# Kernel optimization log

Hardware: AMD Instinct MI355X
Metric: run time of the kernel (lower is better)

The kernel has to match this reference:

```python
import jax, jax.numpy as jnp
import numpy as np

D_IN = 512
D_HID = D_IN // 2  # 256
D_OUT = 3


def setup_inputs() -> dict:
    key = jax.random.key(0)
    k_hs, k_ds, k1, k2, k3, k4 = jax.random.split(key, 6)
    B, L, Tmax = 16, 4096, 512
    hs = jax.random.normal(k_hs, (B, L, D_IN), dtype=jnp.float32)
    ds = jax.random.randint(k_ds, (B, Tmax), 0, 8, dtype=jnp.int64)
    # Linear params stored as (in, out); torch Linear does x @ W.T + b
    s1 = 1.0 / np.sqrt(D_IN)
    s2 = 1.0 / np.sqrt(D_HID)
    W1 = jax.random.uniform(k1, (D_IN, D_HID), jnp.float32, -s1, s1)
    b1 = jax.random.uniform(k2, (D_HID,), jnp.float32, -s1, s1)
    W2 = jax.random.uniform(k3, (D_HID, D_OUT), jnp.float32, -s2, s2)
    b2 = jax.random.uniform(k4, (D_OUT,), jnp.float32, -s2, s2)
    return {"hs": hs, "ds": ds, "W1": W1, "b1": b1, "W2": W2, "b2": b2, "Lmax": 4096}


def _align_durations(hs, ds, Lmax):
    # Vectorized equivalent of the per-element python loop:
    #   d_t = max(floor(ds[b,t] * L / Lmax), 1); segment mean over hs[b, i:i+d_t];
    #   i advances only when ds[b,t] > 0; rows with ds==0 stay zero.
    B, L, D = hs.shape
    mult = L / Lmax
    d = jnp.maximum(jnp.floor(ds.astype(jnp.float32) * mult).astype(jnp.int32), 1)
    valid = ds > 0
    d_eff = jnp.where(valid, d, 0)                      # (B, Tmax)
    starts = jnp.cumsum(d_eff, axis=1) - d_eff          # exclusive cumsum
    ends = starts + d_eff
    s_cl = jnp.clip(starts, 0, L)
    e_cl = jnp.clip(ends, 0, L)
    # prefix sums over frames: P[b, i] = sum of hs[b, :i]
    P = jnp.concatenate(
        [jnp.zeros((B, 1, D), hs.dtype), jnp.cumsum(hs, axis=1)], axis=1
    )  # (B, L+1, D)
    seg_sum = (jnp.take_along_axis(P, e_cl[:, :, None], axis=1)
               - jnp.take_along_axis(P, s_cl[:, :, None], axis=1))  # (B, Tmax, D)
    length = jnp.maximum(e_cl - s_cl, 1).astype(hs.dtype)
    mean = seg_sum / length[:, :, None]
    return jnp.where(valid[:, :, None], mean, jnp.zeros((), hs.dtype))


def reference(hs, ds, W1, b1, W2, b2, Lmax):
    aligned = _align_durations(hs, ds, Lmax)            # (B, Tmax, D_IN)
    # projection MLP (Dropout is identity in eval mode)
    h = jax.nn.relu(jnp.einsum("btd,dh->bth", aligned, W1) + b1)
    out = jax.nn.relu(jnp.einsum("bth,ho->bto", h, W2) + b2)
    return out
```

## Files before the change

### kernel.cpp

```cpp
#include <hip/hip_runtime.h>
#include <math.h>

#define BB    16
#define LL    4096
#define TMAX  512
#define DIN   512
#define DHID  256
#define DOUT  3
#define NROW  (BB * TMAX)
#define RPB   32
#define RPT   8

typedef __attribute__((ext_vector_type(8))) short bf16x8;
typedef __attribute__((ext_vector_type(4))) float f32x4;

static __device__ __forceinline__ ushort f2bf(float x) {
    uint u = __builtin_bit_cast(uint, x);
    u = (u + 0x7FFFu + ((u >> 16) & 1u)) >> 16;
    return (ushort)u;
}


__global__ __launch_bounds__(512) void prep_kernel(
    const int* __restrict__ ds, const int* __restrict__ lmax,
    const float* __restrict__ W1, int* __restrict__ starts,
    int* __restrict__ lens, ushort* __restrict__ pack) {
    __shared__ int   sbuf[TMAX];
    __shared__ float t[64][65];
    const int bid = blockIdx.x;
    const int tid = threadIdx.x;

    if (bid < BB) {
        const int b = bid;
        const float mult = (float)LL / (float)lmax[0];
        const int dsv = ds[b * TMAX + tid];
        int d = (int)floorf((float)dsv * mult);
        d = max(d, 1);
        const int deff = (dsv > 0) ? d : 0;
        sbuf[tid] = deff;
        __syncthreads();
        for (int off = 1; off < TMAX; off <<= 1) {
            int x = (tid >= off) ? sbuf[tid - off] : 0;
            __syncthreads();
            sbuf[tid] += x;
            __syncthreads();
        }
        starts[b * TMAX + tid] = sbuf[tid] - deff;
        lens[b * TMAX + tid]   = deff;
    } else {
        const int tb = bid - BB;
        const int k0 = (tb >> 2) * 64;
        const int n0 = (tb & 3) * 64;
        const int r  = tid >> 3;
        const int c8 = (tid & 7) * 8;
        #pragma unroll
        for (int i = 0; i < 2; ++i) {
            const float4 v =
                *(const float4*)&W1[(size_t)(k0 + r) * DHID + n0 + c8 + i * 4];
            t[r][c8 + i * 4 + 0] = v.x;
            t[r][c8 + i * 4 + 1] = v.y;
            t[r][c8 + i * 4 + 2] = v.z;
            t[r][c8 + i * 4 + 3] = v.w;
        }
        __syncthreads();
        const int col = n0 + r;
        const int kk  = k0 + c8;
        const int nb  = col >> 4;
        const int mm  = col & 15;
        const int ktc = kk >> 5;
        const int gg  = (kk >> 3) & 3;
        ushort tmp[8];
        #pragma unroll
        for (int j = 0; j < 8; ++j) tmp[j] = f2bf(t[c8 + j][r]);
        *(uint4*)&pack[(size_t)(((nb * 16 + ktc) * 64) + gg * 16 + mm) * 8] =
            *(const uint4*)tmp;
    }
}

__global__ __launch_bounds__(512, 2) void fused_kernel(
    const float* __restrict__ hs, const int* __restrict__ starts,
    const int* __restrict__ lens, const ushort* __restrict__ pack,
    const float* __restrict__ b1, const float* __restrict__ W2,
    const float* __restrict__ b2, float* __restrict__ out) {
    __shared__ ushort Asw[RPB * DIN];
    __shared__ float  red[8][RPB][DOUT];

    const int raw  = blockIdx.x;
    const int bid  = (raw & 7) * 32 + (raw >> 3);
    const int row0 = bid * RPB;
    const int b    = row0 >> 9;
    const int tid  = threadIdx.x;
    const int w    = tid >> 6;
    const int l    = tid & 63;
    const int m    = l & 15;
    const int g    = l >> 4;
    const int ct   = tid & 127;
    const int rh   = tid >> 7;

    int s_arr[RPT], n_arr[RPT], last_arr[RPT];
    int nmax = 0;
    #pragma unroll
    for (int rr = 0; rr < RPT; ++rr) {
        const int row = row0 + rh * RPT + rr;
        const int len = lens[row];
        int s = starts[row];
        int e = min(s + len, LL);
        s = min(s, LL);
        const int n = e - s;
        s_arr[rr]    = s;
        n_arr[rr]    = n;
        last_arr[rr] = min(max(e - 1, 0), LL - 1);
        nmax = max(nmax, n);
    }
    float4 a[RPT];
    #pragma unroll
    for (int rr = 0; rr < RPT; ++rr) a[rr] = make_float4(0.f, 0.f, 0.f, 0.f);

    const float* base = hs + (size_t)b * LL * DIN + ct * 4;
    for (int i = 0; i < nmax; ++i) {
        float4 v[RPT];
        #pragma unroll
        for (int rr = 0; rr < RPT; ++rr) {
            const int idx = min(s_arr[rr] + i, last_arr[rr]);
            v[rr] = *(const float4*)(base + (size_t)idx * DIN);
        }
        #pragma unroll
        for (int rr = 0; rr < RPT; ++rr) {
            const bool ok = (i < n_arr[rr]);
            a[rr].x += ok ? v[rr].x : 0.0f;
            a[rr].y += ok ? v[rr].y : 0.0f;
            a[rr].z += ok ? v[rr].z : 0.0f;
            a[rr].w += ok ? v[rr].w : 0.0f;
        }
    }
    #pragma unroll
    for (int rr = 0; rr < RPT; ++rr) {
        const int rl = rh * RPT + rr;
        const float inv = (n_arr[rr] > 0) ? 1.0f / (float)n_arr[rr] : 0.0f;
        ushort4 u;
        u.x = f2bf(a[rr].x * inv);
        u.y = f2bf(a[rr].y * inv);
        u.z = f2bf(a[rr].z * inv);
        u.w = f2bf(a[rr].w * inv);
        *(ushort4*)((char*)Asw + rl * 1024 + ((ct * 8) ^ ((rl & 7) << 4))) = u;
    }
    __syncthreads();

    f32x4 acc00 = {0.f, 0.f, 0.f, 0.f};
    f32x4 acc01 = {0.f, 0.f, 0.f, 0.f};
    f32x4 acc10 = {0.f, 0.f, 0.f, 0.f};
    f32x4 acc11 = {0.f, 0.f, 0.f, 0.f};

    const ushort* bb  = pack + (size_t)l * 8;
    const char* abase0 = (const char*)Asw + m * 1024;
    const char* abase1 = (const char*)Asw + (16 + m) * 1024;
    const int   aswz   = (m & 7) << 4;

    #pragma unroll 4
    for (int ktc = 0; ktc < 16; ++ktc) {
        const bf16x8 bv0 =
            *(const bf16x8*)(bb + (size_t)(((w * 2 + 0) * 16 + ktc) * 512));
        const bf16x8 bv1 =
            *(const bf16x8*)(bb + (size_t)(((w * 2 + 1) * 16 + ktc) * 512));
        const int aoff = (g * 16 + ktc * 64) ^ aswz;
        const bf16x8 av0 = *(const bf16x8*)(abase0 + aoff);
        const bf16x8 av1 = *(const bf16x8*)(abase1 + aoff);
        acc00 = __builtin_amdgcn_mfma_f32_16x16x32_bf16(av0, bv0, acc00, 0, 0, 0);
        acc01 = __builtin_amdgcn_mfma_f32_16x16x32_bf16(av0, bv1, acc01, 0, 0, 0);
        acc10 = __builtin_amdgcn_mfma_f32_16x16x32_bf16(av1, bv0, acc10, 0, 0, 0);
        acc11 = __builtin_amdgcn_mfma_f32_16x16x32_bf16(av1, bv1, acc11, 0, 0, 0);
    }

    float p[2][4][3];
    #pragma unroll
    for (int t = 0; t < 2; ++t)
        #pragma unroll
        for (int r = 0; r < 4; ++r)
            #pragma unroll
            for (int o = 0; o < 3; ++o) p[t][r][o] = 0.0f;

    #pragma unroll
    for (int fc = 0; fc < 2; ++fc) {
        const int col = w * 32 + fc * 16 + m;
        const float bb1 = b1[col];
        const float w20 = W2[col * 3 + 0];
        const float w21 = W2[col * 3 + 1];
        const float w22 = W2[col * 3 + 2];
        const f32x4 a0v = fc ? acc01 : acc00;
        const f32x4 a1v = fc ? acc11 : acc10;
        #pragma unroll
        for (int r = 0; r < 4; ++r) {
            const float h0 = fmaxf(a0v[r] + bb1, 0.0f);
            p[0][r][0] = fmaf(h0, w20, p[0][r][0]);
            p[0][r][1] = fmaf(h0, w21, p[0][r][1]);
            p[0][r][2] = fmaf(h0, w22, p[0][r][2]);
            const float h1 = fmaxf(a1v[r] + bb1, 0.0f);
            p[1][r][0] = fmaf(h1, w20, p[1][r][0]);
            p[1][r][1] = fmaf(h1, w21, p[1][r][1]);
            p[1][r][2] = fmaf(h1, w22, p[1][r][2]);
        }
    }
    #pragma unroll
    for (int mask = 1; mask < 16; mask <<= 1)
        #pragma unroll
        for (int t = 0; t < 2; ++t)
            #pragma unroll
            for (int r = 0; r < 4; ++r)
                #pragma unroll
                for (int o = 0; o < 3; ++o)
                    p[t][r][o] += __shfl_xor(p[t][r][o], mask, 64);

    if (m == 0) {
        #pragma unroll
        for (int t = 0; t < 2; ++t)
            #pragma unroll
            for (int r = 0; r < 4; ++r)
                #pragma unroll
                for (int o = 0; o < 3; ++o)
                    red[w][t * 16 + g * 4 + r][o] = p[t][r][o];
    }
    __syncthreads();

    if (tid < RPB * DOUT) {
        const int rl = tid / 3;
        const int o  = tid % 3;
        float v = b2[o];
        #pragma unroll
        for (int ww = 0; ww < 8; ++ww) v += red[ww][rl][o];
        out[(size_t)(row0 + rl) * DOUT + o] = fmaxf(v, 0.0f);
    }
}

extern "C" void kernel_launch(void* const* d_in, const int* in_sizes, int n_in,
                              void* d_out, int out_size, void* d_ws, size_t ws_size,
                              hipStream_t stream) {
    const float* hs  = (const float*)d_in[0];
    const int*   ds  = (const int*)d_in[1];
    const float* W1  = (const float*)d_in[2];
    const float* b1  = (const float*)d_in[3];
    const float* W2  = (const float*)d_in[4];
    const float* b2  = (const float*)d_in[5];
    const int*   lmx = (const int*)d_in[6];

    char*   wsb    = (char*)d_ws;
    int*    starts = (int*)wsb;
    int*    lens   = (int*)(wsb + 32 * 1024);
    ushort* pack   = (ushort*)(wsb + 64 * 1024);

    prep_kernel<<<BB + 32, 512, 0, stream>>>(ds, lmx, W1, starts, lens, pack);
    fused_kernel<<<NROW / RPB, 512, 0, stream>>>(hs, starts, lens, pack, b1, W2,
                                                 b2, (float*)d_out);
}
```

Measured before the change: 26.55 us.

## Halve rows per block and restructure MFMA tiling for 256-thread blocks

```diff
diff --git a/kernel.cpp b/kernel.cpp
--- a/kernel.cpp
+++ b/kernel.cpp
@@ -8,7 +8,7 @@
 #define DHID  256
 #define DOUT  3
 #define NROW  (BB * TMAX)
-#define RPB   32
+#define RPB   16
 #define RPT   8
 
 typedef __attribute__((ext_vector_type(8))) short bf16x8;
@@ -77,16 +77,16 @@
     }
 }
 
-__global__ __launch_bounds__(512, 2) void fused_kernel(
+__global__ __launch_bounds__(256, 2) void fused_kernel(
     const float* __restrict__ hs, const int* __restrict__ starts,
     const int* __restrict__ lens, const ushort* __restrict__ pack,
     const float* __restrict__ b1, const float* __restrict__ W2,
     const float* __restrict__ b2, float* __restrict__ out) {
     __shared__ ushort Asw[RPB * DIN];
-    __shared__ float  red[8][RPB][DOUT];
+    __shared__ float  red[4][RPB][DOUT];
 
     const int raw  = blockIdx.x;
-    const int bid  = (raw & 7) * 32 + (raw >> 3);
+    const int bid  = (raw & 7) * 64 + (raw >> 3);
     const int row0 = bid * RPB;
     const int b    = row0 >> 9;
     const int tid  = threadIdx.x;
@@ -146,87 +146,69 @@
     }
     __syncthreads();
 
-    f32x4 acc00 = {0.f, 0.f, 0.f, 0.f};
-    f32x4 acc01 = {0.f, 0.f, 0.f, 0.f};
-    f32x4 acc10 = {0.f, 0.f, 0.f, 0.f};
-    f32x4 acc11 = {0.f, 0.f, 0.f, 0.f};
-
-    const ushort* bb  = pack + (size_t)l * 8;
-    const char* abase0 = (const char*)Asw + m * 1024;
-    const char* abase1 = (const char*)Asw + (16 + m) * 1024;
+    f32x4 acc[4] = {{0.f, 0.f, 0.f, 0.f}, {0.f, 0.f, 0.f, 0.f},
+                    {0.f, 0.f, 0.f, 0.f}, {0.f, 0.f, 0.f, 0.f}};
+
+    const ushort* bb   = pack + (size_t)l * 8;
+    const char* abase  = (const char*)Asw + m * 1024;
     const int   aswz   = (m & 7) << 4;
 
     #pragma unroll 4
     for (int ktc = 0; ktc < 16; ++ktc) {
-        const bf16x8 bv0 =
-            *(const bf16x8*)(bb + (size_t)(((w * 2 + 0) * 16 + ktc) * 512));
-        const bf16x8 bv1 =
-            *(const bf16x8*)(bb + (size_t)(((w * 2 + 1) * 16 + ktc) * 512));
         const int aoff = (g * 16 + ktc * 64) ^ aswz;
-        const bf16x8 av0 = *(const bf16x8*)(abase0 + aoff);
-        const bf16x8 av1 = *(const bf16x8*)(abase1 + aoff);
-        acc00 = __builtin_amdgcn_mfma_f32_16x16x32_bf16(av0, bv0, acc00, 0, 0, 0);
-        acc01 = __builtin_amdgcn_mfma_f32_16x16x32_bf16(av0, bv1, acc01, 0, 0, 0);
-        acc10 = __builtin_amdgcn_mfma_f32_16x16x32_bf16(av1, bv0, acc10, 0, 0, 0);
-        acc11 = __builtin_amdgcn_mfma_f32_16x16x32_bf16(av1, bv1, acc11, 0, 0, 0);
-    }
-
-    float p[2][4][3];
-    #pragma unroll
-    for (int t = 0; t < 2; ++t)
-        #pragma unroll
-        for (int r = 0; r < 4; ++r)
-            #pragma unroll
-            for (int o = 0; o < 3; ++o) p[t][r][o] = 0.0f;
-
-    #pragma unroll
-    for (int fc = 0; fc < 2; ++fc) {
-        const int col = w * 32 + fc * 16 + m;
+        const bf16x8 av = *(const bf16x8*)(abase + aoff);
+        #pragma unroll
+        for (int fc = 0; fc < 4; ++fc) {
+            const bf16x8 bv =
+                *(const bf16x8*)(bb + (size_t)(((w * 4 + fc) * 16 + ktc) * 512));
+            acc[fc] = __builtin_amdgcn_mfma_f32_16x16x32_bf16(av, bv, acc[fc],
+                                                              0, 0, 0);
+        }
+    }
+
+    float p[4][3];
+    #pragma unroll
+    for (int r = 0; r < 4; ++r)
+        #pragma unroll
+        for (int o = 0; o < 3; ++o) p[r][o] = 0.0f;
+
+    #pragma unroll
+    for (int fc = 0; fc < 4; ++fc) {
+        const int col = w * 64 + fc * 16 + m;
         const float bb1 = b1[col];
         const float w20 = W2[col * 3 + 0];
         const float w21 = W2[col * 3 + 1];
         const float w22 = W2[col * 3 + 2];
-        const f32x4 a0v = fc ? acc01 : acc00;
-        const f32x4 a1v = fc ? acc11 : acc10;
         #pragma unroll
         for (int r = 0; r < 4; ++r) {
-            const float h0 = fmaxf(a0v[r] + bb1, 0.0f);
-            p[0][r][0] = fmaf(h0, w20, p[0][r][0]);
-            p[0][r][1] = fmaf(h0, w21, p[0][r][1]);
-            p[0][r][2] = fmaf(h0, w22, p[0][r][2]);
-            const float h1 = fmaxf(a1v[r] + bb1, 0.0f);
-            p[1][r][0] = fmaf(h1, w20, p[1][r][0]);
-            p[1][r][1] = fmaf(h1, w21, p[1][r][1]);
-            p[1][r][2] = fmaf(h1, w22, p[1][r][2]);
+            const float h = fmaxf(acc[fc][r] + bb1, 0.0f);
+            p[r][0] = fmaf(h, w20, p[r][0]);
+            p[r][1] = fmaf(h, w21, p[r][1]);
+            p[r][2] = fmaf(h, w22, p[r][2]);
         }
     }
     #pragma unroll
     for (int mask = 1; mask < 16; mask <<= 1)
         #pragma unroll
-        for (int t = 0; t < 2; ++t)
+        for (int r = 0; r < 4; ++r)
             #pragma unroll
-            for (int r = 0; r < 4; ++r)
-                #pragma unroll
-                for (int o = 0; o < 3; ++o)
-                    p[t][r][o] += __shfl_xor(p[t][r][o], mask, 64);
+            for (int o = 0; o < 3; ++o)
+                p[r][o] += __shfl_xor(p[r][o], mask, 64);
 
     if (m == 0) {
         #pragma unroll
-        for (int t = 0; t < 2; ++t)
+        for (int r = 0; r < 4; ++r)
             #pragma unroll
-            for (int r = 0; r < 4; ++r)
-                #pragma unroll
-                for (int o = 0; o < 3; ++o)
-                    red[w][t * 16 + g * 4 + r][o] = p[t][r][o];
+            for (int o = 0; o < 3; ++o)
+                red[w][g * 4 + r][o] = p[r][o];
     }
     __syncthreads();
 
     if (tid < RPB * DOUT) {
         const int rl = tid / 3;
         const int o  = tid % 3;
-        float v = b2[o];
-        #pragma unroll
-        for (int ww = 0; ww < 8; ++ww) v += red[ww][rl][o];
+        const float v = red[0][rl][o] + red[1][rl][o] + red[2][rl][o] +
+                        red[3][rl][o] + b2[o];
         out[(size_t)(row0 + rl) * DOUT + o] = fmaxf(v, 0.0f);
     }
 }
@@ -248,6 +230,6 @@
     ushort* pack   = (ushort*)(wsb + 64 * 1024);
 
     prep_kernel<<<BB + 32, 512, 0, stream>>>(ds, lmx, W1, starts, lens, pack);
-    fused_kernel<<<NROW / RPB, 512, 0, stream>>>(hs, starts, lens, pack, b1, W2,
+    fused_kernel<<<NROW / RPB, 256, 0, stream>>>(hs, starts, lens, pack, b1, W2,
                                                  b2, (float*)d_out);
 }
```

After: 25.99 us. -2.1%, faster.
